# Optimization experiments

Hardware: AMD Instinct MI355X
Metric: run time of the kernel (lower is better)

The kernel has to match this reference:

```python
import jax, jax.numpy as jnp
import numpy as np

VAR_WEIGHT = 1.0
DIST_WEIGHT = 1.0
MARGIN_VAR = 0.5
MARGIN_DIST = 3.0
IGNORE_LABEL = 255
MAX_INST = 12  # static C: max instance id present in gt (labels 1..12, 0=background)


def setup_inputs() -> dict:
    key = jax.random.key(0)
    k1, k2 = jax.random.split(key)
    featmap = jax.random.normal(k1, (8, 16, 368, 640), dtype=jnp.float32)
    gt = jax.random.randint(k2, (8, 1, 368, 640), 0, 13, dtype=jnp.int64)
    return {"featmap": featmap, "gt": gt}


def _push_pull_loss(featmap, gt):
    B, N, H, W = featmap.shape
    P = H * W
    feat = featmap.reshape(B, N, P)                      # [B,N,P]
    labels = gt.reshape(B, P)                            # [B,P] int
    ids = jnp.arange(1, MAX_INST + 1)                    # instance ids 1..C
    # one-hot instance masks  [B,C,P]
    mask = (labels[:, None, :] == ids[None, :, None]).astype(feat.dtype)
    counts = mask.sum(axis=-1)                           # [B,C]
    present = counts > 0                                 # [B,C]
    safe_counts = jnp.maximum(counts, 1.0)
    # per-instance centers (segment mean)  [B,C,N]
    centers = jnp.einsum('bnp,bcp->bcn', feat, mask) / safe_counts[:, :, None]

    # --- pull: per-pixel distance to own-instance center ---
    feat_sq = jnp.sum(feat * feat, axis=1)               # [B,P]
    cen_sq = jnp.sum(centers * centers, axis=-1)         # [B,C]
    cross = jnp.einsum('bcn,bnp->bcp', centers, feat)    # [B,C,P]
    sq = feat_sq[:, None, :] + cen_sq[:, :, None] - 2.0 * cross
    sq = jnp.maximum(sq, 0.0)
    d = jnp.where(sq > 0, jnp.sqrt(jnp.where(sq > 0, sq, 1.0)), 0.0)  # [B,C,P]
    hinge = jnp.maximum(d - MARGIN_VAR, 0.0)
    # per-instance mean over its own pixels
    inst_pull = jnp.sum(hinge * mask, axis=-1) / safe_counts          # [B,C]
    n_inst = jnp.sum(present.astype(feat.dtype))
    pull_loss = jnp.where(
        n_inst > 0,
        jnp.sum(jnp.where(present, inst_pull, 0.0)) / jnp.maximum(n_inst, 1.0),
        0.0 * feat.mean(),
    ) * VAR_WEIGHT

    # --- push: pairwise center distances within each batch sample ---
    diff = centers[:, :, None, :] - centers[:, None, :, :]            # [B,C,C,N]
    psq = jnp.sum(diff * diff, axis=-1)                               # [B,C,C]
    pd = jnp.where(psq > 0, jnp.sqrt(jnp.where(psq > 0, psq, 1.0)), 0.0)
    pair_valid = (present[:, :, None] & present[:, None, :] &
                  (~jnp.eye(MAX_INST, dtype=bool))[None]).astype(feat.dtype)
    push_vals = jnp.maximum(2.0 * MARGIN_DIST - pd, 0.0)
    n_pairs = jnp.sum(pair_valid)
    push_loss = jnp.where(
        n_pairs > 0,
        jnp.sum(push_vals * pair_valid) / jnp.maximum(n_pairs, 1.0),
        0.0 * feat.mean(),
    ) * DIST_WEIGHT

    return push_loss + pull_loss


def reference(featmap, gt):
    return _push_pull_loss(featmap, gt)
```

## Files before the change

kernel.cpp:

```cpp
#include <hip/hip_runtime.h>
#include <hip/hip_bf16.h>

constexpr int B_ = 8;
constexpr int N_ = 16;
constexpr int H_ = 368;
constexpr int W_ = 640;
constexpr int P_ = H_ * W_;
constexpr int C_ = 12;
constexpr float MARGIN_VAR_ = 0.5f;
constexpr float MARGIN_DIST_ = 3.0f;

constexpr int OFF_SUMS = 0;
constexpr int OFF_CNT  = OFF_SUMS + B_*C_*N_;
constexpr int WS_FLOATS = OFF_CNT + B_*C_;

constexpr int TPB = 256;

constexpr int MCHUNK = 1024;
constexpr int MBPI   = P_ / MCHUNK;
constexpr int PCHUNK = 1024;
constexpr int PBPI   = P_ / PCHUNK;

typedef short bf16x8 __attribute__((ext_vector_type(8)));
typedef float f32x4  __attribute__((ext_vector_type(4)));

union FragU { int4 i; bf16x8 v; };

__device__ __forceinline__ short f2bf(float f) {
    __hip_bfloat16 h = __float2bfloat16(f);
    return __builtin_bit_cast(short, h);
}

__device__ __forceinline__ int pack_bf2(float x, float y) {
    const unsigned lo = (unsigned short)f2bf(x);
    const unsigned hi = (unsigned short)f2bf(y);
    return (int)(lo | (hi << 16));
}

__global__ __launch_bounds__(TPB) void k_accum(const float* __restrict__ feat,
                                               const int* __restrict__ gt,
                                               float* __restrict__ ws,
                                               float* __restrict__ out) {
    __shared__ int   s_lab[MCHUNK];
    __shared__ float s_red[4][C_];
    __shared__ float s_fin[4][256];

    const int tid  = threadIdx.x;
    const int lane = tid & 63, wid = tid >> 6;
    const int b     = blockIdx.x / MBPI;
    const int chunk = blockIdx.x % MBPI;
    const int base  = chunk * MCHUNK;

    if (blockIdx.x == 0 && tid == 0) out[0] = 0.f;

    const int*   __restrict__ gb = gt   + (size_t)b * P_ + base;
    const float* __restrict__ fb = feat + (size_t)b * N_ * P_ + base;

    const int4 la = ((const int4*)gb)[tid];
    ((int4*)s_lab)[tid] = la;

    float cnt[C_];
    #pragma unroll
    for (int c = 0; c < C_; ++c) {
        cnt[c] = ((la.x == c+1) ? 1.f : 0.f) + ((la.y == c+1) ? 1.f : 0.f)
               + ((la.z == c+1) ? 1.f : 0.f) + ((la.w == c+1) ? 1.f : 0.f);
    }
    #pragma unroll
    for (int off = 32; off > 0; off >>= 1) {
        #pragma unroll
        for (int c = 0; c < C_; ++c) cnt[c] += __shfl_xor(cnt[c], off, 64);
    }
    if (lane == 0) {
        #pragma unroll
        for (int c = 0; c < C_; ++c) s_red[wid][c] = cnt[c];
    }
    __syncthreads();
    if (tid < C_) {
        const float t = s_red[0][tid] + s_red[1][tid] + s_red[2][tid] + s_red[3][tid];
        atomicAdd(&ws[OFF_CNT + b * C_ + tid], t);
    }

    const int n     = lane & 15;
    const int cls   = n + 1;
    const int ko    = (lane >> 4) * 8;
    const int wbase = wid * 256;
    const float* __restrict__ fp = fb + (size_t)n * P_;

    float4 ba[4], bb[4];
    #pragma unroll
    for (int t = 0; t < 4; ++t) {
        ba[t] = *(const float4*)(fp + wbase + t * 32 + ko);
        bb[t] = *(const float4*)(fp + wbase + t * 32 + ko + 4);
    }

    f32x4 acc = {0.f, 0.f, 0.f, 0.f};

    #pragma unroll
    for (int t = 0; t < 8; ++t) {
        const float4 c0 = ba[t & 3], c1 = bb[t & 3];
        if (t < 4) {
            ba[t & 3] = *(const float4*)(fp + wbase + (t + 4) * 32 + ko);
            bb[t & 3] = *(const float4*)(fp + wbase + (t + 4) * 32 + ko + 4);
        }
        const int* lp = s_lab + wbase + t * 32 + ko;
        const int4 L0 = *(const int4*)(lp);
        const int4 L1 = *(const int4*)(lp + 4);

        FragU au, bu;
        au.i.x = ((L0.x == cls) ? 0x3F80 : 0) | ((L0.y == cls) ? 0x3F800000 : 0);
        au.i.y = ((L0.z == cls) ? 0x3F80 : 0) | ((L0.w == cls) ? 0x3F800000 : 0);
        au.i.z = ((L1.x == cls) ? 0x3F80 : 0) | ((L1.y == cls) ? 0x3F800000 : 0);
        au.i.w = ((L1.z == cls) ? 0x3F80 : 0) | ((L1.w == cls) ? 0x3F800000 : 0);

        bu.i.x = pack_bf2(c0.x, c0.y);
        bu.i.y = pack_bf2(c0.z, c0.w);
        bu.i.z = pack_bf2(c1.x, c1.y);
        bu.i.w = pack_bf2(c1.z, c1.w);

        acc = __builtin_amdgcn_mfma_f32_16x16x32_bf16(au.v, bu.v, acc, 0, 0, 0);
    }

    #pragma unroll
    for (int r = 0; r < 4; ++r) s_fin[wid][lane * 4 + r] = acc[r];
    __syncthreads();

    {
        const float sv = s_fin[0][tid] + s_fin[1][tid] + s_fin[2][tid] + s_fin[3][tid];
        const int elane = tid >> 2, r = tid & 3;
        const int row = (elane >> 4) * 4 + r;
        const int col = elane & 15;
        if (row < C_)
            atomicAdd(&ws[OFF_SUMS + ((size_t)b * C_ + row) * N_ + col], sv);
    }
}

__global__ __launch_bounds__(TPB) void k_pull(const float* __restrict__ feat,
                                              const int* __restrict__ gt,
                                              const float* __restrict__ ws,
                                              float* __restrict__ out) {
    __shared__ float s_cen[C_][N_ + 1];
    __shared__ float s_w[C_];
    __shared__ float s_cntv[B_ * C_];
    __shared__ float red[TPB];
    __shared__ float wsum[TPB / 64];

    const int tid   = threadIdx.x;
    const int b     = blockIdx.x / PBPI;
    const int chunk = blockIdx.x % PBPI;
    const int base  = chunk * PCHUNK;

    const float* __restrict__ fbase = feat + (size_t)b * N_ * P_ + base + tid * 4;

    const int4 lb = *(const int4*)(gt + (size_t)b * P_ + base + tid * 4);
    float4 va[4], vb[4];
    #pragma unroll
    for (int j = 0; j < 4; ++j) va[j] = *(const float4*)(fbase + (size_t)(j) * P_);
    #pragma unroll
    for (int j = 0; j < 4; ++j) vb[j] = *(const float4*)(fbase + (size_t)(4 + j) * P_);

    if (tid < B_ * C_) s_cntv[tid] = ws[OFF_CNT + tid];
    __syncthreads();

    float n_inst = 0.f;
    #pragma unroll 8
    for (int i = 0; i < B_ * C_; ++i) n_inst += (s_cntv[i] > 0.f) ? 1.f : 0.f;

    if (tid < C_ * N_) {
        const int c = tid >> 4, n = tid & 15;
        const float ct = s_cntv[b * C_ + c];
        s_cen[c][n] = ws[OFF_SUMS + ((size_t)b * C_ + c) * N_ + n] / fmaxf(ct, 1.f);
    }
    if (tid < C_) {
        const float ct = s_cntv[b * C_ + tid];
        s_w[tid] = (ct > 0.f && n_inst > 0.f) ? 1.0f / (ct * n_inst) : 0.f;
    }
    __syncthreads();

    if (chunk == 0) {
        float ps = 0.f;
        if (tid < C_ * C_) {
            const int i = tid / C_, j = tid % C_;
            if (i != j && s_cntv[b * C_ + i] > 0.f && s_cntv[b * C_ + j] > 0.f) {
                float sq = 0.f;
                #pragma unroll
                for (int n = 0; n < N_; ++n) {
                    const float d = s_cen[i][n] - s_cen[j][n];
                    sq += d * d;
                }
                ps = fmaxf(2.f * MARGIN_DIST_ - sqrtf(sq), 0.f);
            }
        }
        red[tid] = ps;
        __syncthreads();
        for (int s = TPB / 2; s > 0; s >>= 1) {
            if (tid < s) red[tid] += red[tid + s];
            __syncthreads();
        }
        if (tid == 0) {
            float np = 0.f;
            for (int bb_ = 0; bb_ < B_; ++bb_) {
                int k = 0;
                for (int c = 0; c < C_; ++c) k += (s_cntv[bb_ * C_ + c] > 0.f) ? 1 : 0;
                np += (float)(k * (k - 1));
            }
            if (np > 0.f) atomicAdd(out, red[0] / np);
        }
    }

    const bool vx = (lb.x >= 1 && lb.x <= C_);
    const bool vy = (lb.y >= 1 && lb.y <= C_);
    const bool vz = (lb.z >= 1 && lb.z <= C_);
    const bool vw = (lb.w >= 1 && lb.w <= C_);
    const int cx = vx ? lb.x - 1 : 0;
    const int cy = vy ? lb.y - 1 : 0;
    const int cz = vz ? lb.z - 1 : 0;
    const int cw = vw ? lb.w - 1 : 0;

    float sq0 = 0.f, sq1 = 0.f, sq2 = 0.f, sq3 = 0.f;

    auto consume4 = [&](const float4* r, int cb) {
        #pragma unroll
        for (int j = 0; j < 4; ++j) {
            const int nn = cb + j;
            const float d0 = r[j].x - s_cen[cx][nn];
            const float d1 = r[j].y - s_cen[cy][nn];
            const float d2 = r[j].z - s_cen[cz][nn];
            const float d3 = r[j].w - s_cen[cw][nn];
            sq0 += d0 * d0; sq1 += d1 * d1; sq2 += d2 * d2; sq3 += d3 * d3;
        }
    };

    consume4(va, 0);
    #pragma unroll
    for (int j = 0; j < 4; ++j) va[j] = *(const float4*)(fbase + (size_t)(8 + j) * P_);
    consume4(vb, 4);
    #pragma unroll
    for (int j = 0; j < 4; ++j) vb[j] = *(const float4*)(fbase + (size_t)(12 + j) * P_);
    consume4(va, 8);
    consume4(vb, 12);

    float acc = 0.f;
    acc += fmaxf(sqrtf(sq0) - MARGIN_VAR_, 0.f) * (vx ? s_w[cx] : 0.f);
    acc += fmaxf(sqrtf(sq1) - MARGIN_VAR_, 0.f) * (vy ? s_w[cy] : 0.f);
    acc += fmaxf(sqrtf(sq2) - MARGIN_VAR_, 0.f) * (vz ? s_w[cz] : 0.f);
    acc += fmaxf(sqrtf(sq3) - MARGIN_VAR_, 0.f) * (vw ? s_w[cw] : 0.f);

    #pragma unroll
    for (int off = 32; off > 0; off >>= 1) acc += __shfl_down(acc, off, 64);
    const int lane = tid & 63, wid = tid >> 6;
    if (lane == 0) wsum[wid] = acc;
    __syncthreads();
    if (tid == 0) {
        float t = 0.f;
        #pragma unroll
        for (int w = 0; w < TPB / 64; ++w) t += wsum[w];
        atomicAdd(out, t);
    }
}

extern "C" void kernel_launch(void* const* d_in, const int* in_sizes, int n_in,
                              void* d_out, int out_size, void* d_ws, size_t ws_size,
                              hipStream_t stream) {
    const float* feat = (const float*)d_in[0];
    const int*   gt   = (const int*)d_in[1];
    float* out = (float*)d_out;
    float* ws  = (float*)d_ws;

    (void)hipMemsetAsync(d_ws, 0, WS_FLOATS * sizeof(float), stream);

    k_accum<<<dim3(B_ * MBPI), dim3(TPB), 0, stream>>>(feat, gt, ws, out);
    k_pull <<<dim3(B_ * PBPI), dim3(TPB), 0, stream>>>(feat, gt, ws, out);
}
```

Baseline: 70.49 us.

## Stage features as bf16 in LDS and reverse pull-kernel block order for cache reuse

The accumulation kernel now loads all 16 feature rows of its chunk with coalesced float4 loads, converts them to bf16 and stores them in shared memory. MFMA B fragments are then read from LDS instead of being gathered from global memory with strided loads. The pull kernel visits blocks in reverse group order so it first touches data the previous kernel read last, aiming to hit in the large last-level cache. The larger shared-memory footprint may lower occupancy.

```diff
diff --git a/kernel.cpp b/kernel.cpp
--- a/kernel.cpp
+++ b/kernel.cpp
@@ -20,6 +20,9 @@
 constexpr int MBPI   = P_ / MCHUNK;
 constexpr int PCHUNK = 1024;
 constexpr int PBPI   = P_ / PCHUNK;
+constexpr int NBLK   = B_ * PBPI;
+
+constexpr int ROWS_ = 1048;
 
 typedef short bf16x8 __attribute__((ext_vector_type(8)));
 typedef float f32x4  __attribute__((ext_vector_type(4)));
@@ -42,6 +45,7 @@
                                                float* __restrict__ ws,
                                                float* __restrict__ out) {
     __shared__ int   s_lab[MCHUNK];
+    __shared__ short s_feat[N_ * ROWS_];
     __shared__ float s_red[4][C_];
     __shared__ float s_fin[4][256];
 
@@ -59,6 +63,24 @@
     const int4 la = ((const int4*)gb)[tid];
     ((int4*)s_lab)[tid] = la;
 
+    float4 g[8];
+    #pragma unroll
+    for (int j = 0; j < 8; ++j)
+        g[j] = *(const float4*)(fb + (size_t)j * P_ + tid * 4);
+    #pragma unroll
+    for (int j = 0; j < 8; ++j) {
+        const float4 v = g[j];
+        g[j] = *(const float4*)(fb + (size_t)(8 + j) * P_ + tid * 4);
+        int2 w; w.x = pack_bf2(v.x, v.y); w.y = pack_bf2(v.z, v.w);
+        *(int2*)(s_feat + j * ROWS_ + tid * 4) = w;
+    }
+    #pragma unroll
+    for (int j = 0; j < 8; ++j) {
+        const float4 v = g[j];
+        int2 w; w.x = pack_bf2(v.x, v.y); w.y = pack_bf2(v.z, v.w);
+        *(int2*)(s_feat + (8 + j) * ROWS_ + tid * 4) = w;
+    }
+
     float cnt[C_];
     #pragma unroll
     for (int c = 0; c < C_; ++c) {
@@ -80,29 +102,18 @@
         atomicAdd(&ws[OFF_CNT + b * C_ + tid], t);
     }
 
-    const int n     = lane & 15;
-    const int cls   = n + 1;
-    const int ko    = (lane >> 4) * 8;
-    const int wbase = wid * 256;
-    const float* __restrict__ fp = fb + (size_t)n * P_;
-
-    float4 ba[4], bb[4];
-    #pragma unroll
-    for (int t = 0; t < 4; ++t) {
-        ba[t] = *(const float4*)(fp + wbase + t * 32 + ko);
-        bb[t] = *(const float4*)(fp + wbase + t * 32 + ko + 4);
-    }
+    const int n   = lane & 15;
+    const int cls = n + 1;
+    const int ko  = (lane >> 4) * 8;
+
+    const short* __restrict__ bp = s_feat + n * ROWS_ + ko;
 
     f32x4 acc = {0.f, 0.f, 0.f, 0.f};
 
     #pragma unroll
-    for (int t = 0; t < 8; ++t) {
-        const float4 c0 = ba[t & 3], c1 = bb[t & 3];
-        if (t < 4) {
-            ba[t & 3] = *(const float4*)(fp + wbase + (t + 4) * 32 + ko);
-            bb[t & 3] = *(const float4*)(fp + wbase + (t + 4) * 32 + ko + 4);
-        }
-        const int* lp = s_lab + wbase + t * 32 + ko;
+    for (int k = 0; k < 8; ++k) {
+        const int t = wid * 8 + k;
+        const int* lp = s_lab + t * 32 + ko;
         const int4 L0 = *(const int4*)(lp);
         const int4 L1 = *(const int4*)(lp + 4);
 
@@ -112,10 +123,7 @@
         au.i.z = ((L1.x == cls) ? 0x3F80 : 0) | ((L1.y == cls) ? 0x3F800000 : 0);
         au.i.w = ((L1.z == cls) ? 0x3F80 : 0) | ((L1.w == cls) ? 0x3F800000 : 0);
 
-        bu.i.x = pack_bf2(c0.x, c0.y);
-        bu.i.y = pack_bf2(c0.z, c0.w);
-        bu.i.z = pack_bf2(c1.x, c1.y);
-        bu.i.w = pack_bf2(c1.z, c1.w);
+        bu.v = *(const bf16x8*)(bp + t * 32);
 
         acc = __builtin_amdgcn_mfma_f32_16x16x32_bf16(au.v, bu.v, acc, 0, 0, 0);
     }
@@ -144,9 +152,10 @@
     __shared__ float red[TPB];
     __shared__ float wsum[TPB / 64];
 
-    const int tid   = threadIdx.x;
-    const int b     = blockIdx.x / PBPI;
-    const int chunk = blockIdx.x % PBPI;
+    const int tid = threadIdx.x;
+    const int g2    = (NBLK / 8 - 1 - (int)(blockIdx.x >> 3)) * 8 + (blockIdx.x & 7);
+    const int b     = g2 / PBPI;
+    const int chunk = g2 % PBPI;
     const int base  = chunk * PCHUNK;
 
     const float* __restrict__ fbase = feat + (size_t)b * N_ * P_ + base + tid * 4;
@@ -269,5 +278,5 @@
     (void)hipMemsetAsync(d_ws, 0, WS_FLOATS * sizeof(float), stream);
 
     k_accum<<<dim3(B_ * MBPI), dim3(TPB), 0, stream>>>(feat, gt, ws, out);
-    k_pull <<<dim3(B_ * PBPI), dim3(TPB), 0, stream>>>(feat, gt, ws, out);
-}
+    k_pull <<<dim3(NBLK), dim3(TPB), 0, stream>>>(feat, gt, ws, out);
+}
```

After: 68.82 us. 1.02x faster.
